# Kernel tuning notes

Hardware: AMD Instinct MI355X
Metric: run time of the kernel (lower is better)

## Reference

```python
import jax, jax.numpy as jnp
import numpy as np

N_USERS = 100000
N_ITEMS = 50000
N_NODES = N_USERS + N_ITEMS
N_EDGES = 4800000
EMB = 64
N_LAYERS = 3
BATCH = 16384


def setup_inputs() -> dict:
    key = jax.random.key(0)
    ks = jax.random.split(key, 12)
    users = jax.random.randint(ks[0], (BATCH,), 0, N_USERS)
    pos_items = jax.random.randint(ks[1], (BATCH,), 0, N_ITEMS)
    neg_items = jax.random.randint(ks[2], (BATCH,), 0, N_ITEMS)
    rows = jax.random.randint(ks[3], (N_EDGES,), 0, N_NODES)
    cols = jax.random.randint(ks[4], (N_EDGES,), 0, N_NODES)
    vals = jax.random.uniform(ks[5], (N_EDGES,), dtype=jnp.float32)
    # learned parameters (xavier-ish scale)
    user_emb = jax.random.normal(ks[6], (N_USERS, EMB), dtype=jnp.float32) * 0.1
    item_emb = jax.random.normal(ks[7], (N_ITEMS, EMB), dtype=jnp.float32) * 0.1
    # Linear weights stored as [in, out] so y = x @ W + b (matches torch Linear math)
    W1s = jax.random.normal(ks[8], (N_LAYERS, EMB, EMB), dtype=jnp.float32) * (1.0 / np.sqrt(EMB))
    b1s = jnp.zeros((N_LAYERS, EMB), dtype=jnp.float32)
    W2s = jax.random.normal(ks[9], (N_LAYERS, EMB, EMB), dtype=jnp.float32) * (1.0 / np.sqrt(EMB))
    b2s = jnp.zeros((N_LAYERS, EMB), dtype=jnp.float32)
    return dict(users=users, pos_items=pos_items, neg_items=neg_items,
                rows=rows, cols=cols, vals=vals,
                user_emb=user_emb, item_emb=item_emb,
                W1s=W1s, b1s=b1s, W2s=W2s, b2s=b2s)


def _leaky_relu(x):
    return jnp.where(x > 0, x, 0.2 * x)


def _computer(user_emb, item_emb, rows, cols, vals, W1s, b1s, W2s, b2s):
    all_emb = jnp.concatenate([user_emb, item_emb], axis=0)  # [N, 64]
    embs = [all_emb]
    for i in range(N_LAYERS):
        self_emb = all_emb @ W1s[i] + b1s[i]
        # sparse adjacency SpMM: gather neighbor features, weight, segment-sum by row
        neighbor = jax.ops.segment_sum(vals[:, None] * all_emb[cols], rows,
                                       num_segments=N_NODES)
        neighbor = neighbor @ W2s[i] + b2s[i]
        interact = (neighbor * all_emb) @ W2s[i] + b2s[i]
        all_emb = _leaky_relu(self_emb + neighbor + interact)
        embs.append(all_emb)
    embs = jnp.concatenate(embs, axis=1)  # [N, 64*(n_layers+1)] = [N, 256]
    return embs[:N_USERS], embs[N_USERS:]


def reference(users, pos_items, neg_items, rows, cols, vals,
              user_emb, item_emb, W1s, b1s, W2s, b2s):
    all_users, all_items = _computer(user_emb, item_emb, rows, cols, vals,
                                     W1s, b1s, W2s, b2s)
    users_emb = all_users[users]
    pos_emb = all_items[pos_items]
    neg_emb = all_items[neg_items]
    return users_emb, pos_emb, neg_emb
```

## Files before the change

kernel.cpp:

```cpp
#include <hip/hip_runtime.h>


#define EMB 64

constexpr int kNUsers = 100000;
constexpr int kNItems = 50000;
constexpr int kNNodes = 150000;
constexpr int kNEdges = 4800000;
constexpr int kBatch  = 16384;
constexpr int kLayers = 3;
constexpr int kRngShift = 8;
constexpr int kNRanges  = (kNNodes + 255) >> 8;
constexpr int kEdgesPerBin = 16384;
constexpr int kBinBlocks = (kNEdges + kEdgesPerBin - 1) / kEdgesPerBin;
constexpr int kEPW    = 16;

__device__ __forceinline__ float f4c(const float4& v, int i) {
  return ((const float*)&v)[i];
}
__device__ __forceinline__ float4 f4fma(float s, float4 w, float4 a) {
  a.x = fmaf(s, w.x, a.x);
  a.y = fmaf(s, w.y, a.y);
  a.z = fmaf(s, w.z, a.z);
  a.w = fmaf(s, w.w, a.w);
  return a;
}
__device__ __forceinline__ float4 f4add(float4 a, float4 b) {
  a.x += b.x; a.y += b.y; a.z += b.z; a.w += b.w;
  return a;
}
__device__ __forceinline__ float lrelu(float x) { return x > 0.f ? x : 0.2f * x; }
__device__ __forceinline__ unsigned short f2bf(float f) {
  unsigned int u = __float_as_uint(f);
  u = (u + 0x7fffu + ((u >> 16) & 1u)) >> 16;
  return (unsigned short)u;
}
__device__ __forceinline__ float bf2f(unsigned short h) {
  return __uint_as_float(((unsigned int)h) << 16);
}

#define F16(M) M(0) M(1) M(2) M(3) M(4) M(5) M(6) M(7) \
               M(8) M(9) M(10) M(11) M(12) M(13) M(14) M(15)

__global__ __launch_bounds__(256) void init_embed(
    const float* __restrict__ user_emb, const float* __restrict__ item_emb,
    float* __restrict__ cur, unsigned short* __restrict__ cur16, int with16)
{
  const size_t userF = (size_t)kNUsers * EMB;
  const size_t allF4 = (size_t)kNNodes * EMB / 4;
  const size_t i = (size_t)blockIdx.x * 256 + threadIdx.x;
  if (i >= allF4) return;
  const size_t f = i * 4;
  const float4 v = (f < userF) ? ((const float4*)user_emb)[i]
                               : ((const float4*)(item_emb))[(f - userF) / 4];
  ((float4*)cur)[i] = v;
  if (with16) {
    ushort4 h;
    h.x = f2bf(v.x); h.y = f2bf(v.y); h.z = f2bf(v.z); h.w = f2bf(v.w);
    ((ushort4*)cur16)[i] = h;
  }
}

__global__ __launch_bounds__(256) void refresh16(
    const float* __restrict__ cur, unsigned short* __restrict__ cur16)
{
  const size_t allF4 = (size_t)kNNodes * EMB / 4;
  const size_t i = (size_t)blockIdx.x * 256 + threadIdx.x;
  if (i >= allF4) return;
  const float4 v = ((const float4*)cur)[i];
  ushort4 h;
  h.x = f2bf(v.x); h.y = f2bf(v.y); h.z = f2bf(v.z); h.w = f2bf(v.w);
  ((ushort4*)cur16)[i] = h;
}


__global__ __launch_bounds__(256) void hist_ranges(
    const int* __restrict__ rows, int* __restrict__ rangeA)
{
  __shared__ int cnt[kNRanges];
  const int tid = threadIdx.x;
  const int e0  = blockIdx.x * kEdgesPerBin;
  int e1 = e0 + kEdgesPerBin;
  if (e1 > kNEdges) e1 = kNEdges;
  for (int b = tid; b < kNRanges; b += 256) cnt[b] = 0;
  __syncthreads();
  for (int e = e0 + tid; e < e1; e += 256)
    atomicAdd(&cnt[rows[e] >> kRngShift], 1);
  __syncthreads();
  for (int b = tid; b < kNRanges; b += 256)
    if (cnt[b] > 0) atomicAdd(&rangeA[b], cnt[b]);
}

__global__ __launch_bounds__(1024) void scan_ranges(
    int* __restrict__ rangeA, int* __restrict__ rowPtr)
{
  __shared__ int wsum[16];
  const int tid  = threadIdx.x;
  const int lane = tid & 63;
  const int wid  = tid >> 6;
  const int cnt  = (tid < kNRanges) ? rangeA[tid] : 0;
  int v = cnt;
#pragma unroll
  for (int off = 1; off < 64; off <<= 1) {
    const int n = __shfl_up(v, off, 64);
    if (lane >= off) v += n;
  }
  if (lane == 63) wsum[wid] = v;
  __syncthreads();
  if (tid == 0) {
    int s = 0;
#pragma unroll
    for (int w = 0; w < 16; ++w) { const int t = wsum[w]; wsum[w] = s; s += t; }
  }
  __syncthreads();
  if (tid < kNRanges) rangeA[tid] = wsum[wid] + v - cnt;
  if (tid == 0) {
    rangeA[kNRanges]  = kNEdges;
    rowPtr[kNNodes]   = kNEdges;
  }
}

__global__ __launch_bounds__(256) void bin_edges(
    const int* __restrict__ rows, const int* __restrict__ cols,
    const float* __restrict__ vals, const int* __restrict__ rangeA,
    int* __restrict__ rangeCnt, int2* __restrict__ tmpE)
{
  __shared__ int cnt[kNRanges];
  __shared__ int base[kNRanges];
  const int tid = threadIdx.x;
  const int e0  = blockIdx.x * kEdgesPerBin;
  int e1 = e0 + kEdgesPerBin;
  if (e1 > kNEdges) e1 = kNEdges;

  for (int b = tid; b < kNRanges; b += 256) cnt[b] = 0;
  __syncthreads();
  for (int e = e0 + tid; e < e1; e += 256)
    atomicAdd(&cnt[rows[e] >> kRngShift], 1);
  __syncthreads();
  for (int b = tid; b < kNRanges; b += 256) {
    const int c = cnt[b];
    base[b] = (c > 0) ? (rangeA[b] + atomicAdd(&rangeCnt[b], c)) : 0;
    cnt[b] = 0;
  }
  __syncthreads();
  for (int e = e0 + tid; e < e1; e += 256) {
    const int r = rows[e];
    const int b = r >> kRngShift;
    const int rank = atomicAdd(&cnt[b], 1);
    tmpE[base[b] + rank] =
        make_int2(cols[e] | ((r & 255) << 18), __float_as_int(vals[e]));
  }
}

__global__ __launch_bounds__(256) void place_edges(
    const int2* __restrict__ tmpE, const int* __restrict__ rangeA,
    int2* __restrict__ edgeS, int* __restrict__ rowPtr)
{
  __shared__ int lcnt[256];
  __shared__ int lbase[256];
  __shared__ int ws[4];
  const int b    = blockIdx.x;
  const int r0   = b << kRngShift;
  const int tid  = threadIdx.x;
  const int lane = tid & 63;
  const int wid  = tid >> 6;
  const int start = rangeA[b];
  const int end   = rangeA[b + 1];

  lcnt[tid] = 0;
  __syncthreads();
  for (int e = start + tid; e < end; e += 256)
    atomicAdd(&lcnt[(tmpE[e].x >> 18) & 255], 1);
  __syncthreads();

  const int c = lcnt[tid];
  int v = c;
#pragma unroll
  for (int off = 1; off < 64; off <<= 1) {
    const int n = __shfl_up(v, off, 64);
    if (lane >= off) v += n;
  }
  if (lane == 63) ws[wid] = v;
  __syncthreads();
  int wadd = 0;
#pragma unroll
  for (int w = 0; w < 4; ++w) if (w < wid) wadd += ws[w];
  const int excl = v - c + wadd;
  lbase[tid] = start + excl;
  if (r0 + tid < kNNodes) rowPtr[r0 + tid] = start + excl;
  lcnt[tid] = 0;
  __syncthreads();

  for (int e = start + tid; e < end; e += 256) {
    const int2 cv = tmpE[e];
    const int rl  = (cv.x >> 18) & 255;
    const int rank = atomicAdd(&lcnt[rl], 1);
    edgeS[lbase[rl] + rank] = make_int2(cv.x & 0x3FFFF, cv.y);
  }
}

__global__ __launch_bounds__(256) void spmm_csr16(
    const unsigned short* __restrict__ cur16, const int* __restrict__ rowPtr,
    const int2* __restrict__ edgeS, float* __restrict__ nbuf)
{
  const int lane = threadIdx.x & 63;
  const int r = (blockIdx.x << 2) | (threadIdx.x >> 6);
  if (r >= kNNodes) return;
  const int start = __builtin_amdgcn_readfirstlane(rowPtr[r]);
  const int end   = __builtin_amdgcn_readfirstlane(rowPtr[r + 1]);
  float a0 = 0.f, a1 = 0.f, a2 = 0.f, a3 = 0.f;
  int e = start;
  for (; e + 4 <= end; e += 4) {
    const int2 cv0 = edgeS[e];
    const int2 cv1 = edgeS[e + 1];
    const int2 cv2 = edgeS[e + 2];
    const int2 cv3 = edgeS[e + 3];
    const unsigned short u0 = cur16[(size_t)cv0.x * EMB + lane];
    const unsigned short u1 = cur16[(size_t)cv1.x * EMB + lane];
    const unsigned short u2 = cur16[(size_t)cv2.x * EMB + lane];
    const unsigned short u3 = cur16[(size_t)cv3.x * EMB + lane];
    a0 = fmaf(__int_as_float(cv0.y), bf2f(u0), a0);
    a1 = fmaf(__int_as_float(cv1.y), bf2f(u1), a1);
    a2 = fmaf(__int_as_float(cv2.y), bf2f(u2), a2);
    a3 = fmaf(__int_as_float(cv3.y), bf2f(u3), a3);
  }
  for (; e < end; ++e) {
    const int2 cv = edgeS[e];
    a0 = fmaf(__int_as_float(cv.y), bf2f(cur16[(size_t)cv.x * EMB + lane]), a0);
  }
  nbuf[(size_t)r * EMB + lane] = (a0 + a1) + (a2 + a3);
}

__global__ __launch_bounds__(256) void spmm_csr(
    const float* __restrict__ cur, const int* __restrict__ rowPtr,
    const int2* __restrict__ edgeS, float* __restrict__ nbuf)
{
  const int lane = threadIdx.x & 63;
  const int r = (blockIdx.x << 2) | (threadIdx.x >> 6);
  if (r >= kNNodes) return;
  const int start = __builtin_amdgcn_readfirstlane(rowPtr[r]);
  const int end   = __builtin_amdgcn_readfirstlane(rowPtr[r + 1]);
  float a0 = 0.f, a1 = 0.f, a2 = 0.f, a3 = 0.f;
  int e = start;
  for (; e + 4 <= end; e += 4) {
    const int2 cv0 = edgeS[e];
    const int2 cv1 = edgeS[e + 1];
    const int2 cv2 = edgeS[e + 2];
    const int2 cv3 = edgeS[e + 3];
    a0 = fmaf(__int_as_float(cv0.y), cur[(size_t)cv0.x * EMB + lane], a0);
    a1 = fmaf(__int_as_float(cv1.y), cur[(size_t)cv1.x * EMB + lane], a1);
    a2 = fmaf(__int_as_float(cv2.y), cur[(size_t)cv2.x * EMB + lane], a2);
    a3 = fmaf(__int_as_float(cv3.y), cur[(size_t)cv3.x * EMB + lane], a3);
  }
  for (; e < end; ++e) {
    const int2 cv = edgeS[e];
    a0 = fmaf(__int_as_float(cv.y), cur[(size_t)cv.x * EMB + lane], a0);
  }
  nbuf[(size_t)r * EMB + lane] = (a0 + a1) + (a2 + a3);
}

__global__ __launch_bounds__(256) void spmm_atomic(
    const float* __restrict__ cur, const int* __restrict__ rows,
    const int* __restrict__ cols, const float* __restrict__ vals,
    float* __restrict__ nbuf)
{
  const int lane = threadIdx.x & 63;
  int wv = (blockIdx.x << 2) | (threadIdx.x >> 6);
  wv = __builtin_amdgcn_readfirstlane(wv);
  int e0 = wv * kEPW;
  int e1 = e0 + kEPW;
  if (e1 > kNEdges) e1 = kNEdges;
  for (int e = e0; e < e1; ++e) {
    atomicAdd(nbuf + (size_t)rows[e] * EMB + lane,
              vals[e] * cur[(size_t)cols[e] * EMB + lane]);
  }
}

__global__ __launch_bounds__(256) void transform_nbr(
    float* __restrict__ nbuf, const float* __restrict__ W2,
    const float* __restrict__ b2)
{
  const int node = blockIdx.x * 256 + threadIdx.x;
  if (node >= kNNodes) return;
  const float4* __restrict__ nr  = (const float4*)(nbuf + (size_t)node * EMB);
  const float4* __restrict__ b2v = (const float4*)b2;
#define DECL(j) float4 a##j = b2v[j];
  F16(DECL)
#undef DECL
#pragma unroll 4
  for (int k4 = 0; k4 < 16; ++k4) {
    const float4 nv = nr[k4];
#pragma unroll
    for (int kk = 0; kk < 4; ++kk) {
      const float ns = f4c(nv, kk);
      const float4* __restrict__ w2r = (const float4*)(W2 + (4 * k4 + kk) * EMB);
#define STEP(j) a##j = f4fma(ns, w2r[j], a##j);
      F16(STEP)
#undef STEP
    }
  }
  float4* __restrict__ outp = (float4*)(nbuf + (size_t)node * EMB);
#define STORE(j) outp[j] = a##j;
  F16(STORE)
#undef STORE
}

__global__ __launch_bounds__(256) void transform_self(
    float* __restrict__ cur, const float* __restrict__ nbuf,
    const float* __restrict__ W1, const float* __restrict__ b1,
    const float* __restrict__ b2, const float* __restrict__ W2)
{
  const int node = blockIdx.x * 256 + threadIdx.x;
  if (node >= kNNodes) return;
  const float4* __restrict__ xr  = (const float4*)(cur  + (size_t)node * EMB);
  const float4* __restrict__ tr  = (const float4*)(nbuf + (size_t)node * EMB);
  const float4* __restrict__ b1v = (const float4*)b1;
  const float4* __restrict__ b2v = (const float4*)b2;
#define DECL(j) float4 a##j = f4add(b1v[j], b2v[j]);
  F16(DECL)
#undef DECL
#pragma unroll 2
  for (int k4 = 0; k4 < 16; ++k4) {
    const float4 xv = xr[k4];
    const float4 tv = tr[k4];
#pragma unroll
    for (int kk = 0; kk < 4; ++kk) {
      const float xs = f4c(xv, kk);
      const float ms = f4c(tv, kk) * xs;
      const int k = 4 * k4 + kk;
      const float4* __restrict__ w1r = (const float4*)(W1 + k * EMB);
      const float4* __restrict__ w2r = (const float4*)(W2 + k * EMB);
#define STEP(j) a##j = f4fma(xs, w1r[j], a##j); a##j = f4fma(ms, w2r[j], a##j);
      F16(STEP)
#undef STEP
    }
  }
  float4* __restrict__ outp = (float4*)(cur + (size_t)node * EMB);
#define STORE(j) { const float4 tj = tr[j]; float4 r;          \
    r.x = lrelu(a##j.x + tj.x); r.y = lrelu(a##j.y + tj.y);    \
    r.z = lrelu(a##j.z + tj.z); r.w = lrelu(a##j.w + tj.w);    \
    outp[j] = r; }
  F16(STORE)
#undef STORE
}

__global__ __launch_bounds__(256) void gather_out(
    const float* __restrict__ cur, const int* __restrict__ users,
    const int* __restrict__ pos, const int* __restrict__ neg,
    float* __restrict__ out, int layer)
{
  const int t    = blockIdx.x * 256 + threadIdx.x;
  const int lane = t & 63;
  const int rid  = t >> 6;
  if (rid >= 3 * kBatch) return;
  const int seg = rid / kBatch;
  const int b   = rid - seg * kBatch;
  int idx;
  if (seg == 0)      idx = users[b];
  else if (seg == 1) idx = pos[b] + kNUsers;
  else               idx = neg[b] + kNUsers;
  out[(size_t)rid * 256 + layer * EMB + lane] = cur[(size_t)idx * EMB + lane];
}

extern "C" void kernel_launch(void* const* d_in, const int* in_sizes, int n_in,
                              void* d_out, int out_size, void* d_ws, size_t ws_size,
                              hipStream_t stream) {
  const int*   users    = (const int*)d_in[0];
  const int*   pos      = (const int*)d_in[1];
  const int*   neg      = (const int*)d_in[2];
  const int*   rows     = (const int*)d_in[3];
  const int*   cols     = (const int*)d_in[4];
  const float* vals     = (const float*)d_in[5];
  const float* user_emb = (const float*)d_in[6];
  const float* item_emb = (const float*)d_in[7];
  const float* W1s      = (const float*)d_in[8];
  const float* b1s      = (const float*)d_in[9];
  const float* W2s      = (const float*)d_in[10];
  const float* b2s      = (const float*)d_in[11];
  float* out = (float*)d_out;

  const size_t nodeF = (size_t)kNNodes * EMB;
  float* cur  = (float*)d_ws;
  float* nbuf = cur + nodeF;
  int2*  edgeS     = (int2*)(nbuf + nodeF);
  int*   rowPtr    = (int*)(edgeS + kNEdges);
  int*   rangeA    = rowPtr + (kNNodes + 1);
  int*   rangeCnt  = rangeA + (kNRanges + 1);
  unsigned short* cur16 = (unsigned short*)(rangeCnt + kNRanges);
  int2*  tmpE = (int2*)nbuf;
  const size_t neededCsr = (size_t)((char*)cur16 - (char*)d_ws);
  const size_t needed16  = neededCsr + nodeF * sizeof(unsigned short);
  const bool useCsr = ws_size >= neededCsr;
  const bool use16  = useCsr && ws_size >= needed16;

  const dim3 blk(256);
  const int iblocks = (int)((nodeF / 4 + 255) / 256);
  const int gblocks = (3 * kBatch * EMB + 255) / 256;
  const int rblocks = (kNNodes + 3) / 4;
  const int tblocks = (kNNodes + 255) / 256;

  init_embed<<<iblocks, blk, 0, stream>>>(user_emb, item_emb, cur, cur16,
                                          use16 ? 1 : 0);

  if (useCsr) {
    hipMemsetAsync(rangeA, 0, (size_t)(2 * kNRanges + 1) * sizeof(int), stream);
    hist_ranges<<<kBinBlocks, blk, 0, stream>>>(rows, rangeA);
    scan_ranges<<<1, 1024, 0, stream>>>(rangeA, rowPtr);
    bin_edges<<<kBinBlocks, blk, 0, stream>>>(rows, cols, vals, rangeA,
                                              rangeCnt, tmpE);
    place_edges<<<kNRanges, blk, 0, stream>>>(tmpE, rangeA, edgeS, rowPtr);
  }

  gather_out<<<gblocks, blk, 0, stream>>>(cur, users, pos, neg, out, 0);

  for (int L = 0; L < kLayers; ++L) {
    if (useCsr) {
      if (use16)
        spmm_csr16<<<rblocks, blk, 0, stream>>>(cur16, rowPtr, edgeS, nbuf);
      else
        spmm_csr<<<rblocks, blk, 0, stream>>>(cur, rowPtr, edgeS, nbuf);
    } else {
      hipMemsetAsync(nbuf, 0, nodeF * sizeof(float), stream);
      const int sblocks = (((kNEdges + kEPW - 1) / kEPW) + 3) / 4;
      spmm_atomic<<<sblocks, blk, 0, stream>>>(cur, rows, cols, vals, nbuf);
    }
    transform_nbr<<<tblocks, blk, 0, stream>>>(
        nbuf, W2s + L * EMB * EMB, b2s + L * EMB);
    transform_self<<<tblocks, blk, 0, stream>>>(
        cur, nbuf, W1s + L * EMB * EMB, b1s + L * EMB,
        b2s + L * EMB, W2s + L * EMB * EMB);
    if (use16 && L + 1 < kLayers)
      refresh16<<<iblocks, blk, 0, stream>>>(cur, cur16);
    gather_out<<<gblocks, blk, 0, stream>>>(cur, users, pos, neg, out, L + 1);
  }
}
```

Measured before the change: 1.312 ms.

## Sub-bucket CSR edges by column range and widen binning blocks

In place_edges, edges within each row are now also grouped into column buckets of 8192 nodes, using per-row, per-bucket shared counters. Each row's neighbor list therefore comes out roughly sorted by column, which should give the SpMM gathers from the bf16 embedding table more locality in cache. The histogram and binning kernels are also launched with 1024 threads instead of 256. The costs are more shared memory per place_edges block (256×19 ints) and extra per-thread prefix work.

```diff
diff --git a/kernel.cpp b/kernel.cpp
--- a/kernel.cpp
+++ b/kernel.cpp
@@ -13,6 +13,8 @@
 constexpr int kNRanges  = (kNNodes + 255) >> 8;
 constexpr int kEdgesPerBin = 16384;
 constexpr int kBinBlocks = (kNEdges + kEdgesPerBin - 1) / kEdgesPerBin;
+constexpr int kBktShift = 13;
+constexpr int kNBkt     = (kNNodes + 8191) >> 13;
 constexpr int kEPW    = 16;
 
 __device__ __forceinline__ float f4c(const float4& v, int i) {
@@ -74,7 +76,7 @@
 }
 
 
-__global__ __launch_bounds__(256) void hist_ranges(
+__global__ __launch_bounds__(1024) void hist_ranges(
     const int* __restrict__ rows, int* __restrict__ rangeA)
 {
   __shared__ int cnt[kNRanges];
@@ -82,12 +84,12 @@
   const int e0  = blockIdx.x * kEdgesPerBin;
   int e1 = e0 + kEdgesPerBin;
   if (e1 > kNEdges) e1 = kNEdges;
-  for (int b = tid; b < kNRanges; b += 256) cnt[b] = 0;
-  __syncthreads();
-  for (int e = e0 + tid; e < e1; e += 256)
+  for (int b = tid; b < kNRanges; b += 1024) cnt[b] = 0;
+  __syncthreads();
+  for (int e = e0 + tid; e < e1; e += 1024)
     atomicAdd(&cnt[rows[e] >> kRngShift], 1);
   __syncthreads();
-  for (int b = tid; b < kNRanges; b += 256)
+  for (int b = tid; b < kNRanges; b += 1024)
     if (cnt[b] > 0) atomicAdd(&rangeA[b], cnt[b]);
 }
 
@@ -120,7 +122,7 @@
   }
 }
 
-__global__ __launch_bounds__(256) void bin_edges(
+__global__ __launch_bounds__(1024) void bin_edges(
     const int* __restrict__ rows, const int* __restrict__ cols,
     const float* __restrict__ vals, const int* __restrict__ rangeA,
     int* __restrict__ rangeCnt, int2* __restrict__ tmpE)
@@ -132,18 +134,18 @@
   int e1 = e0 + kEdgesPerBin;
   if (e1 > kNEdges) e1 = kNEdges;
 
-  for (int b = tid; b < kNRanges; b += 256) cnt[b] = 0;
-  __syncthreads();
-  for (int e = e0 + tid; e < e1; e += 256)
+  for (int b = tid; b < kNRanges; b += 1024) cnt[b] = 0;
+  __syncthreads();
+  for (int e = e0 + tid; e < e1; e += 1024)
     atomicAdd(&cnt[rows[e] >> kRngShift], 1);
   __syncthreads();
-  for (int b = tid; b < kNRanges; b += 256) {
+  for (int b = tid; b < kNRanges; b += 1024) {
     const int c = cnt[b];
     base[b] = (c > 0) ? (rangeA[b] + atomicAdd(&rangeCnt[b], c)) : 0;
     cnt[b] = 0;
   }
   __syncthreads();
-  for (int e = e0 + tid; e < e1; e += 256) {
+  for (int e = e0 + tid; e < e1; e += 1024) {
     const int r = rows[e];
     const int b = r >> kRngShift;
     const int rank = atomicAdd(&cnt[b], 1);
@@ -156,8 +158,7 @@
     const int2* __restrict__ tmpE, const int* __restrict__ rangeA,
     int2* __restrict__ edgeS, int* __restrict__ rowPtr)
 {
-  __shared__ int lcnt[256];
-  __shared__ int lbase[256];
+  __shared__ int bcnt[256][kNBkt];
   __shared__ int ws[4];
   const int b    = blockIdx.x;
   const int r0   = b << kRngShift;
@@ -167,13 +168,18 @@
   const int start = rangeA[b];
   const int end   = rangeA[b + 1];
 
-  lcnt[tid] = 0;
-  __syncthreads();
-  for (int e = start + tid; e < end; e += 256)
-    atomicAdd(&lcnt[(tmpE[e].x >> 18) & 255], 1);
-  __syncthreads();
-
-  const int c = lcnt[tid];
+#pragma unroll
+  for (int k = 0; k < kNBkt; ++k) bcnt[tid][k] = 0;
+  __syncthreads();
+  for (int e = start + tid; e < end; e += 256) {
+    const int cv = tmpE[e].x;
+    atomicAdd(&bcnt[(cv >> 18) & 255][(cv & 0x3FFFF) >> kBktShift], 1);
+  }
+  __syncthreads();
+
+  int c = 0;
+#pragma unroll
+  for (int k = 0; k < kNBkt; ++k) c += bcnt[tid][k];
   int v = c;
 #pragma unroll
   for (int off = 1; off < 64; off <<= 1) {
@@ -185,17 +191,23 @@
   int wadd = 0;
 #pragma unroll
   for (int w = 0; w < 4; ++w) if (w < wid) wadd += ws[w];
-  const int excl = v - c + wadd;
-  lbase[tid] = start + excl;
-  if (r0 + tid < kNNodes) rowPtr[r0 + tid] = start + excl;
-  lcnt[tid] = 0;
+  const int rbase = start + v - c + wadd;
+  if (r0 + tid < kNNodes) rowPtr[r0 + tid] = rbase;
+  int off = rbase;
+#pragma unroll
+  for (int k = 0; k < kNBkt; ++k) {
+    const int t = bcnt[tid][k];
+    bcnt[tid][k] = off;
+    off += t;
+  }
   __syncthreads();
 
   for (int e = start + tid; e < end; e += 256) {
     const int2 cv = tmpE[e];
     const int rl  = (cv.x >> 18) & 255;
-    const int rank = atomicAdd(&lcnt[rl], 1);
-    edgeS[lbase[rl] + rank] = make_int2(cv.x & 0x3FFFF, cv.y);
+    const int col = cv.x & 0x3FFFF;
+    const int slot = atomicAdd(&bcnt[rl][col >> kBktShift], 1);
+    edgeS[slot] = make_int2(col, cv.y);
   }
 }
 
@@ -404,10 +416,10 @@
 
   if (useCsr) {
     hipMemsetAsync(rangeA, 0, (size_t)(2 * kNRanges + 1) * sizeof(int), stream);
-    hist_ranges<<<kBinBlocks, blk, 0, stream>>>(rows, rangeA);
+    hist_ranges<<<kBinBlocks, dim3(1024), 0, stream>>>(rows, rangeA);
     scan_ranges<<<1, 1024, 0, stream>>>(rangeA, rowPtr);
-    bin_edges<<<kBinBlocks, blk, 0, stream>>>(rows, cols, vals, rangeA,
-                                              rangeCnt, tmpE);
+    bin_edges<<<kBinBlocks, dim3(1024), 0, stream>>>(rows, cols, vals, rangeA,
+                                                     rangeCnt, tmpE);
     place_edges<<<kNRanges, blk, 0, stream>>>(tmpE, rangeA, edgeS, rowPtr);
   }
 
```

Measured after the change: 1.283 ms. -2.2%, faster.

## Quantize gathered embeddings to int8 with per-row scales for SpMM

Applied to the files above, without the earlier changes.

Replaces the bf16 copy of node embeddings used in the SpMM gather with an int8 copy plus a per-row float scale computed by a wave-level max reduction. This halves the bytes gathered per edge from the random-access embedding table, at the cost of an extra scale load per edge and coarser precision that could break accuracy tolerances. The edge-binning and histogram kernels also move from 256-thread to 1024-thread blocks.

```diff
diff --git a/kernel.cpp b/kernel.cpp
--- a/kernel.cpp
+++ b/kernel.cpp
@@ -30,21 +30,13 @@
   return a;
 }
 __device__ __forceinline__ float lrelu(float x) { return x > 0.f ? x : 0.2f * x; }
-__device__ __forceinline__ unsigned short f2bf(float f) {
-  unsigned int u = __float_as_uint(f);
-  u = (u + 0x7fffu + ((u >> 16) & 1u)) >> 16;
-  return (unsigned short)u;
-}
-__device__ __forceinline__ float bf2f(unsigned short h) {
-  return __uint_as_float(((unsigned int)h) << 16);
-}
 
 #define F16(M) M(0) M(1) M(2) M(3) M(4) M(5) M(6) M(7) \
                M(8) M(9) M(10) M(11) M(12) M(13) M(14) M(15)
 
 __global__ __launch_bounds__(256) void init_embed(
     const float* __restrict__ user_emb, const float* __restrict__ item_emb,
-    float* __restrict__ cur, unsigned short* __restrict__ cur16, int with16)
+    float* __restrict__ cur)
 {
   const size_t userF = (size_t)kNUsers * EMB;
   const size_t allF4 = (size_t)kNNodes * EMB / 4;
@@ -54,27 +46,27 @@
   const float4 v = (f < userF) ? ((const float4*)user_emb)[i]
                                : ((const float4*)(item_emb))[(f - userF) / 4];
   ((float4*)cur)[i] = v;
-  if (with16) {
-    ushort4 h;
-    h.x = f2bf(v.x); h.y = f2bf(v.y); h.z = f2bf(v.z); h.w = f2bf(v.w);
-    ((ushort4*)cur16)[i] = h;
-  }
-}
-
-__global__ __launch_bounds__(256) void refresh16(
-    const float* __restrict__ cur, unsigned short* __restrict__ cur16)
-{
-  const size_t allF4 = (size_t)kNNodes * EMB / 4;
-  const size_t i = (size_t)blockIdx.x * 256 + threadIdx.x;
-  if (i >= allF4) return;
-  const float4 v = ((const float4*)cur)[i];
-  ushort4 h;
-  h.x = f2bf(v.x); h.y = f2bf(v.y); h.z = f2bf(v.z); h.w = f2bf(v.w);
-  ((ushort4*)cur16)[i] = h;
-}
-
-
-__global__ __launch_bounds__(256) void hist_ranges(
+}
+
+__global__ __launch_bounds__(256) void quant8(
+    const float* __restrict__ cur, signed char* __restrict__ cur8,
+    float* __restrict__ rowScale)
+{
+  const int lane = threadIdx.x & 63;
+  const int r = (blockIdx.x << 2) | (threadIdx.x >> 6);
+  if (r >= kNNodes) return;
+  const float v = cur[(size_t)r * EMB + lane];
+  float m = fabsf(v);
+#pragma unroll
+  for (int off = 32; off >= 1; off >>= 1)
+    m = fmaxf(m, __shfl_xor(m, off, 64));
+  const float inv = (m > 0.f) ? (127.0f / m) : 0.f;
+  cur8[(size_t)r * EMB + lane] = (signed char)__float2int_rn(v * inv);
+  if (lane == 0) rowScale[r] = m * (1.0f / 127.0f);
+}
+
+
+__global__ __launch_bounds__(1024) void hist_ranges(
     const int* __restrict__ rows, int* __restrict__ rangeA)
 {
   __shared__ int cnt[kNRanges];
@@ -82,12 +74,12 @@
   const int e0  = blockIdx.x * kEdgesPerBin;
   int e1 = e0 + kEdgesPerBin;
   if (e1 > kNEdges) e1 = kNEdges;
-  for (int b = tid; b < kNRanges; b += 256) cnt[b] = 0;
-  __syncthreads();
-  for (int e = e0 + tid; e < e1; e += 256)
+  for (int b = tid; b < kNRanges; b += 1024) cnt[b] = 0;
+  __syncthreads();
+  for (int e = e0 + tid; e < e1; e += 1024)
     atomicAdd(&cnt[rows[e] >> kRngShift], 1);
   __syncthreads();
-  for (int b = tid; b < kNRanges; b += 256)
+  for (int b = tid; b < kNRanges; b += 1024)
     if (cnt[b] > 0) atomicAdd(&rangeA[b], cnt[b]);
 }
 
@@ -120,7 +112,7 @@
   }
 }
 
-__global__ __launch_bounds__(256) void bin_edges(
+__global__ __launch_bounds__(1024) void bin_edges(
     const int* __restrict__ rows, const int* __restrict__ cols,
     const float* __restrict__ vals, const int* __restrict__ rangeA,
     int* __restrict__ rangeCnt, int2* __restrict__ tmpE)
@@ -132,18 +124,18 @@
   int e1 = e0 + kEdgesPerBin;
   if (e1 > kNEdges) e1 = kNEdges;
 
-  for (int b = tid; b < kNRanges; b += 256) cnt[b] = 0;
-  __syncthreads();
-  for (int e = e0 + tid; e < e1; e += 256)
+  for (int b = tid; b < kNRanges; b += 1024) cnt[b] = 0;
+  __syncthreads();
+  for (int e = e0 + tid; e < e1; e += 1024)
     atomicAdd(&cnt[rows[e] >> kRngShift], 1);
   __syncthreads();
-  for (int b = tid; b < kNRanges; b += 256) {
+  for (int b = tid; b < kNRanges; b += 1024) {
     const int c = cnt[b];
     base[b] = (c > 0) ? (rangeA[b] + atomicAdd(&rangeCnt[b], c)) : 0;
     cnt[b] = 0;
   }
   __syncthreads();
-  for (int e = e0 + tid; e < e1; e += 256) {
+  for (int e = e0 + tid; e < e1; e += 1024) {
     const int r = rows[e];
     const int b = r >> kRngShift;
     const int rank = atomicAdd(&cnt[b], 1);
@@ -199,9 +191,10 @@
   }
 }
 
-__global__ __launch_bounds__(256) void spmm_csr16(
-    const unsigned short* __restrict__ cur16, const int* __restrict__ rowPtr,
-    const int2* __restrict__ edgeS, float* __restrict__ nbuf)
+__global__ __launch_bounds__(256) void spmm_csr8(
+    const signed char* __restrict__ cur8, const float* __restrict__ rowScale,
+    const int* __restrict__ rowPtr, const int2* __restrict__ edgeS,
+    float* __restrict__ nbuf)
 {
   const int lane = threadIdx.x & 63;
   const int r = (blockIdx.x << 2) | (threadIdx.x >> 6);
@@ -215,18 +208,23 @@
     const int2 cv1 = edgeS[e + 1];
     const int2 cv2 = edgeS[e + 2];
     const int2 cv3 = edgeS[e + 3];
-    const unsigned short u0 = cur16[(size_t)cv0.x * EMB + lane];
-    const unsigned short u1 = cur16[(size_t)cv1.x * EMB + lane];
-    const unsigned short u2 = cur16[(size_t)cv2.x * EMB + lane];
-    const unsigned short u3 = cur16[(size_t)cv3.x * EMB + lane];
-    a0 = fmaf(__int_as_float(cv0.y), bf2f(u0), a0);
-    a1 = fmaf(__int_as_float(cv1.y), bf2f(u1), a1);
-    a2 = fmaf(__int_as_float(cv2.y), bf2f(u2), a2);
-    a3 = fmaf(__int_as_float(cv3.y), bf2f(u3), a3);
+    const int q0 = cur8[(size_t)cv0.x * EMB + lane];
+    const int q1 = cur8[(size_t)cv1.x * EMB + lane];
+    const int q2 = cur8[(size_t)cv2.x * EMB + lane];
+    const int q3 = cur8[(size_t)cv3.x * EMB + lane];
+    const float s0 = __int_as_float(cv0.y) * rowScale[cv0.x];
+    const float s1 = __int_as_float(cv1.y) * rowScale[cv1.x];
+    const float s2 = __int_as_float(cv2.y) * rowScale[cv2.x];
+    const float s3 = __int_as_float(cv3.y) * rowScale[cv3.x];
+    a0 = fmaf(s0, (float)q0, a0);
+    a1 = fmaf(s1, (float)q1, a1);
+    a2 = fmaf(s2, (float)q2, a2);
+    a3 = fmaf(s3, (float)q3, a3);
   }
   for (; e < end; ++e) {
     const int2 cv = edgeS[e];
-    a0 = fmaf(__int_as_float(cv.y), bf2f(cur16[(size_t)cv.x * EMB + lane]), a0);
+    const int q = cur8[(size_t)cv.x * EMB + lane];
+    a0 = fmaf(__int_as_float(cv.y) * rowScale[cv.x], (float)q, a0);
   }
   nbuf[(size_t)r * EMB + lane] = (a0 + a1) + (a2 + a3);
 }
@@ -386,12 +384,13 @@
   int*   rowPtr    = (int*)(edgeS + kNEdges);
   int*   rangeA    = rowPtr + (kNNodes + 1);
   int*   rangeCnt  = rangeA + (kNRanges + 1);
-  unsigned short* cur16 = (unsigned short*)(rangeCnt + kNRanges);
+  signed char* cur8 = (signed char*)(rangeCnt + kNRanges);
+  float* rowScale  = (float*)(cur8 + nodeF);
   int2*  tmpE = (int2*)nbuf;
-  const size_t neededCsr = (size_t)((char*)cur16 - (char*)d_ws);
-  const size_t needed16  = neededCsr + nodeF * sizeof(unsigned short);
+  const size_t neededCsr = (size_t)((char*)cur8 - (char*)d_ws);
+  const size_t needed8   = (size_t)((char*)(rowScale + kNNodes) - (char*)d_ws);
   const bool useCsr = ws_size >= neededCsr;
-  const bool use16  = useCsr && ws_size >= needed16;
+  const bool use8   = useCsr && ws_size >= needed8;
 
   const dim3 blk(256);
   const int iblocks = (int)((nodeF / 4 + 255) / 256);
@@ -399,15 +398,16 @@
   const int rblocks = (kNNodes + 3) / 4;
   const int tblocks = (kNNodes + 255) / 256;
 
-  init_embed<<<iblocks, blk, 0, stream>>>(user_emb, item_emb, cur, cur16,
-                                          use16 ? 1 : 0);
+  init_embed<<<iblocks, blk, 0, stream>>>(user_emb, item_emb, cur);
+  if (use8)
+    quant8<<<rblocks, blk, 0, stream>>>(cur, cur8, rowScale);
 
   if (useCsr) {
     hipMemsetAsync(rangeA, 0, (size_t)(2 * kNRanges + 1) * sizeof(int), stream);
-    hist_ranges<<<kBinBlocks, blk, 0, stream>>>(rows, rangeA);
+    hist_ranges<<<kBinBlocks, dim3(1024), 0, stream>>>(rows, rangeA);
     scan_ranges<<<1, 1024, 0, stream>>>(rangeA, rowPtr);
-    bin_edges<<<kBinBlocks, blk, 0, stream>>>(rows, cols, vals, rangeA,
-                                              rangeCnt, tmpE);
+    bin_edges<<<kBinBlocks, dim3(1024), 0, stream>>>(rows, cols, vals, rangeA,
+                                                     rangeCnt, tmpE);
     place_edges<<<kNRanges, blk, 0, stream>>>(tmpE, rangeA, edgeS, rowPtr);
   }
 
@@ -415,8 +415,9 @@
 
   for (int L = 0; L < kLayers; ++L) {
     if (useCsr) {
-      if (use16)
-        spmm_csr16<<<rblocks, blk, 0, stream>>>(cur16, rowPtr, edgeS, nbuf);
+      if (use8)
+        spmm_csr8<<<rblocks, blk, 0, stream>>>(cur8, rowScale, rowPtr, edgeS,
+                                               nbuf);
       else
         spmm_csr<<<rblocks, blk, 0, stream>>>(cur, rowPtr, edgeS, nbuf);
     } else {
@@ -429,8 +430,8 @@
     transform_self<<<tblocks, blk, 0, stream>>>(
         cur, nbuf, W1s + L * EMB * EMB, b1s + L * EMB,
         b2s + L * EMB, W2s + L * EMB * EMB);
-    if (use16 && L + 1 < kLayers)
-      refresh16<<<iblocks, blk, 0, stream>>>(cur, cur16);
+    if (use8 && L + 1 < kLayers)
+      quant8<<<rblocks, blk, 0, stream>>>(cur, cur8, rowScale);
     gather_out<<<gblocks, blk, 0, stream>>>(cur, users, pos, neg, out, L + 1);
   }
 }
```

Result: slower. 1.340 ms (+2.1%).
